# Performance work log

Hardware: AMD Instinct MI355X
Metric: run time of the kernel (lower is better)

Reference implementation:

```python
import jax, jax.numpy as jnp
import numpy as np
import math

B, S, D, H = 16, 1024, 1024, 16
HD = D // H                      # 64 head dim
MLP_H = int(int(D * 4.0) * 2 / 3)  # 2730 SwiGLU hidden
EPS = 1e-6


def _rmsnorm(h, w):
    # fp32 RMSNorm over last dim
    v = jnp.mean(h * h, axis=-1, keepdims=True)
    return w * (h * jax.lax.rsqrt(v + EPS))


def _rope(x):
    # x: [B, H, S, HD]; standard rotary, half-split convention
    hd = x.shape[-1]
    pos = jnp.arange(x.shape[-2], dtype=jnp.float32)
    inv = 1.0 / (10000.0 ** (jnp.arange(0, hd, 2, dtype=jnp.float32) / hd))
    fr = pos[:, None] * inv[None, :]          # [S, HD/2]
    cos, sin = jnp.cos(fr), jnp.sin(fr)
    x1, x2 = jnp.split(x, 2, axis=-1)
    return jnp.concatenate([x1 * cos - x2 * sin, x1 * sin + x2 * cos], axis=-1)


def setup_inputs() -> dict:
    key = jax.random.key(0)
    ks = jax.random.split(key, 16)
    sc = 0.02
    return {
        "x": jax.random.normal(ks[0], (B, S, D), jnp.float32),
        "c": jax.random.normal(ks[1], (B, D), jnp.float32),
        "w_qkv": jax.random.normal(ks[2], (D, 3 * D), jnp.float32) * sc,
        "b_qkv": jnp.zeros((3 * D,), jnp.float32),
        "w_proj": jax.random.normal(ks[3], (D, D), jnp.float32) * sc,
        "b_proj": jnp.zeros((D,), jnp.float32),
        "w12": jax.random.normal(ks[4], (D, 2 * MLP_H), jnp.float32) * sc,
        "b12": jnp.zeros((2 * MLP_H,), jnp.float32),
        "w3": jax.random.normal(ks[5], (MLP_H, D), jnp.float32) * sc,
        "b3": jnp.zeros((D,), jnp.float32),
        "w_ada": jax.random.normal(ks[6], (D, 6 * D), jnp.float32) * sc,
        "b_ada": jnp.zeros((6 * D,), jnp.float32),
        "norm1_w": jnp.ones((D,), jnp.float32),
        "norm2_w": jnp.ones((D,), jnp.float32),
        "qn_w": jnp.ones((HD,), jnp.float32),
        "kn_w": jnp.ones((HD,), jnp.float32),
    }


def _forward(x, c, w_qkv, b_qkv, w_proj, b_proj, w12, b12, w3, b3,
             w_ada, b_ada, norm1_w, norm2_w, qn_w, kn_w):
    # adaLN modulation params
    ada = jax.nn.silu(c) @ w_ada + b_ada               # [B, 6D]
    sh_a, sc_a, g_a, sh_m, sc_m, g_m = jnp.split(ada, 6, axis=-1)

    def modulate(h, shift, scale):
        return h * (1.0 + scale[:, None, :]) + shift[:, None, :]

    # --- attention branch ---
    h = modulate(_rmsnorm(x, norm1_w), sh_a, sc_a)     # [B, S, D]
    qkv = (h @ w_qkv + b_qkv).reshape(B, S, 3, H, HD)
    qkv = jnp.transpose(qkv, (2, 0, 3, 1, 4))          # [3, B, H, S, HD]
    q, k, v = qkv[0], qkv[1], qkv[2]
    q = _rope(_rmsnorm(q, qn_w))
    k = _rope(_rmsnorm(k, kn_w))
    scores = jnp.einsum('bhqd,bhkd->bhqk', q, k) / math.sqrt(HD)
    attn = jax.nn.softmax(scores, axis=-1)
    o = jnp.einsum('bhqk,bhkd->bhqd', attn, v)         # [B, H, S, HD]
    o = jnp.transpose(o, (0, 2, 1, 3)).reshape(B, S, D)
    o = o @ w_proj + b_proj
    x = x + g_a[:, None, :] * o

    # --- SwiGLU MLP branch ---
    h = modulate(_rmsnorm(x, norm2_w), sh_m, sc_m)
    x12 = h @ w12 + b12
    x1, x2 = jnp.split(x12, 2, axis=-1)
    mlp = (jax.nn.silu(x1) * x2) @ w3 + b3
    return x + g_m[:, None, :] * mlp


def reference(x, c, w_qkv, b_qkv, w_proj, b_proj, w12, b12, w3, b3,
              w_ada, b_ada, norm1_w, norm2_w, qn_w, kn_w):
    return _forward(x, c, w_qkv, b_qkv, w_proj, b_proj, w12, b12, w3, b3,
                    w_ada, b_ada, norm1_w, norm2_w, qn_w, kn_w)
```

## Files before the change

kernel.cpp:

```cpp
#include <hip/hip_runtime.h>
#include <hip/hip_bf16.h>
#include <math.h>

namespace {

constexpr int Bb = 16;
constexpr int Ss = 1024;
constexpr int Dd = 1024;
constexpr int Hh = 16;
constexpr int HD = 64;
constexpr int MLPH = 2730;
constexpr int MLPH_PAD = 2752;
constexpr int ADA_LD = 6144;
constexpr int NR = Bb * Ss;

typedef __attribute__((ext_vector_type(8))) short bf16x8;
typedef __attribute__((ext_vector_type(4))) float f32x4;
typedef __hip_bfloat16 bf16;
typedef unsigned int u32;

__device__ __forceinline__ float bf2f(bf16 v){ return __bfloat162float(v); }
__device__ __forceinline__ bf16 f2bf(float v){ return __float2bfloat16(v); }
__device__ __forceinline__ short f2bfs(float v){ bf16 t = __float2bfloat16(v); return __builtin_bit_cast(short, t); }

__device__ __forceinline__ f32x4 mfma16(bf16x8 a, bf16x8 b, f32x4 c){
  return __builtin_amdgcn_mfma_f32_16x16x32_bf16(a, b, c, 0, 0, 0);
}

__device__ __forceinline__ void gload16(const void* g, void* l){
  __builtin_amdgcn_global_load_lds(
      (const __attribute__((address_space(1))) u32*)g,
      (__attribute__((address_space(3))) u32*)l, 16, 0, 0);
}

__device__ __forceinline__ bf16x8 dsr128(const short* p){
  f32x4 r;
  asm volatile("ds_read_b128 %0, %1" : "=v"(r) : "v"((u32)(size_t)p));
  return __builtin_bit_cast(bf16x8, r);
}


__global__ void k_silu(const float* __restrict__ c, float* __restrict__ out, int n){
  int i = blockIdx.x*256 + threadIdx.x;
  if(i < n){ float v = c[i]; out[i] = v / (1.f + __expf(-v)); }
}

__global__ __launch_bounds__(256) void k_ada(const float* __restrict__ sc,
    const float* __restrict__ w, const float* __restrict__ bias, float* __restrict__ ada){
  __shared__ float red[4][Bb][64];
  int tid = threadIdx.x;
  int jj = tid & 63, ks = tid >> 6;
  int j = blockIdx.x*64 + jj;
  float acc[Bb];
  #pragma unroll
  for(int b=0;b<Bb;++b) acc[b] = 0.f;
  for(int k=ks*256; k<ks*256+256; ++k){
    float wv = w[(size_t)k*ADA_LD + j];
    #pragma unroll
    for(int b=0;b<Bb;++b) acc[b] += sc[b*Dd + k] * wv;
  }
  #pragma unroll
  for(int b=0;b<Bb;++b) red[ks][b][jj] = acc[b];
  __syncthreads();
  #pragma unroll
  for(int rep=0;rep<4;++rep){
    int idx = rep*256 + tid;
    int b = idx >> 6, j2 = idx & 63;
    float s = red[0][b][j2]+red[1][b][j2]+red[2][b][j2]+red[3][b][j2];
    ada[(size_t)b*ADA_LD + blockIdx.x*64 + j2] = s + bias[blockIdx.x*64 + j2];
  }
}

__global__ void k_rope_tab(float2* __restrict__ tab){
  int i = blockIdx.x*256 + threadIdx.x;
  int s = i >> 5, f = i & 31;
  float inv = powf(10000.f, -((float)(2*f)) / 64.f);
  float fr = (float)s * inv;
  float sv, cv;
  sincosf(fr, &sv, &cv);
  tab[i] = make_float2(cv, sv);
}

__global__ void k_transpose(const float* __restrict__ in, bf16* __restrict__ out,
                            int R, int C, int Rpad){
  __shared__ short tile[32][33];
  int tx = threadIdx.x & 31, ty = threadIdx.x >> 5;
  int tr0 = blockIdx.x*32, tc0 = blockIdx.y*32;
  #pragma unroll
  for(int i=0;i<4;++i){
    int r = tr0 + ty + i*8, cc = tc0 + tx;
    short v = 0;
    if(r < R && cc < C) v = f2bfs(in[(size_t)r*C + cc]);
    tile[ty+i*8][tx] = v;
  }
  __syncthreads();
  #pragma unroll
  for(int i=0;i<4;++i){
    int oc = tc0 + ty + i*8;
    int orow = tr0 + tx;
    if(oc < C && orow < Rpad)
      out[(size_t)oc*Rpad + orow] = __builtin_bit_cast(bf16, tile[tx][ty+i*8]);
  }
}

__global__ __launch_bounds__(256) void k_norm_mod(const float* __restrict__ x,
    const float* __restrict__ w, const float* __restrict__ shift, const float* __restrict__ scale,
    bf16* __restrict__ out){
  int r = blockIdx.x;
  int b = r >> 10;
  int t = threadIdx.x;
  const float* xr = x + (size_t)r*Dd;
  float v[4]; float ss = 0.f;
  #pragma unroll
  for(int i=0;i<4;++i){
    float f = xr[t*4+i];
    v[i] = f; ss += f*f;
  }
  #pragma unroll
  for(int m=1;m<64;m<<=1) ss += __shfl_xor(ss, m);
  __shared__ float red[4];
  if((t & 63) == 0) red[t>>6] = ss;
  __syncthreads();
  float tot = red[0]+red[1]+red[2]+red[3];
  float rms = rsqrtf(tot * (1.f/Dd) + 1e-6f);
  #pragma unroll
  for(int i=0;i<4;++i){
    int ccol = t*4+i;
    float h = v[i]*rms*w[ccol];
    float scv = scale[(size_t)b*ADA_LD + ccol];
    float shv = shift[(size_t)b*ADA_LD + ccol];
    out[(size_t)r*Dd + ccol] = f2bf(h*(1.f+scv) + shv);
  }
}

__global__ __launch_bounds__(256) void k_qknorm(bf16* __restrict__ qkv,
    const float* __restrict__ qw, const float* __restrict__ kw,
    const float2* __restrict__ tab){
  int bs = blockIdx.x;
  int s = bs & (Ss-1);
  int tid = threadIdx.x;
  int wv = tid >> 6, lane = tid & 63;
  int isK = wv >> 1;
  int chunk = (wv & 1)*64 + lane;
  int c = chunk & 7;
  int h = chunk >> 3;
  int dih = c*8;
  bf16* p = qkv + (size_t)bs*3072 + isK*Dd + h*HD + dih;
  bf16x8 v = *(const bf16x8*)p;
  float x[8]; float ss = 0.f;
  #pragma unroll
  for(int i=0;i<8;++i){ x[i] = bf2f(__builtin_bit_cast(bf16,(short)v[i])); ss += x[i]*x[i]; }
  ss += __shfl_xor(ss,1); ss += __shfl_xor(ss,2); ss += __shfl_xor(ss,4);
  float rms = rsqrtf(ss*(1.f/HD) + 1e-6f);
  const float* wn = isK ? kw : qw;
  float xn[8];
  #pragma unroll
  for(int i=0;i<8;++i) xn[i] = x[i]*rms*wn[dih+i];
  u32 pk[4], pq[4];
  #pragma unroll
  for(int i=0;i<4;++i)
    pk[i] = (u32)(unsigned short)f2bfs(xn[2*i]) |
            ((u32)(unsigned short)f2bfs(xn[2*i+1]) << 16);
  #pragma unroll
  for(int i=0;i<4;++i) pq[i] = __shfl_xor((int)pk[i], 4);
  float px[8];
  #pragma unroll
  for(int i=0;i<4;++i){
    px[2*i]   = bf2f(__builtin_bit_cast(bf16,(short)(pq[i] & 0xffff)));
    px[2*i+1] = bf2f(__builtin_bit_cast(bf16,(short)(pq[i] >> 16)));
  }
  const float2* tb = tab + s*32 + (c & 3)*8;
  float qs = isK ? 1.f : 0.18033688f;
  bf16x8 o;
  #pragma unroll
  for(int i=0;i<8;++i){
    float2 cs = tb[i];
    float r = (c < 4) ? (xn[i]*cs.x - px[i]*cs.y) : (px[i]*cs.y + xn[i]*cs.x);
    o[i] = f2bfs(r*qs);
  }
  *(bf16x8*)p = o;
}

#define LDA8(M,KH) dsr128(&Ah[((M)*16 + l15)*64 + ((((KH)*4 + l4) ^ l7))*8])
#define PHASE8(M0, STAGE_STMT, GATE_STMT) do{ \
  bf16x8 a0k0 = LDA8(M0,0), a0k1 = LDA8(M0,1), a1k0 = LDA8(M0+1,0), a1k1 = LDA8(M0+1,1); \
  STAGE_STMT; \
  __builtin_amdgcn_s_barrier(); \
  asm volatile("s_waitcnt lgkmcnt(0)" ::: "memory"); \
  __builtin_amdgcn_sched_barrier(0); \
  __builtin_amdgcn_s_setprio(1); \
  acc[M0][0]=mfma16(a0k0,bfrag[0][0],acc[M0][0]); \
  acc[M0][1]=mfma16(a0k0,bfrag[1][0],acc[M0][1]); \
  acc[M0][2]=mfma16(a0k0,bfrag[2][0],acc[M0][2]); \
  acc[M0][3]=mfma16(a0k0,bfrag[3][0],acc[M0][3]); \
  acc[M0+1][0]=mfma16(a1k0,bfrag[0][0],acc[M0+1][0]); \
  acc[M0+1][1]=mfma16(a1k0,bfrag[1][0],acc[M0+1][1]); \
  acc[M0+1][2]=mfma16(a1k0,bfrag[2][0],acc[M0+1][2]); \
  acc[M0+1][3]=mfma16(a1k0,bfrag[3][0],acc[M0+1][3]); \
  acc[M0][0]=mfma16(a0k1,bfrag[0][1],acc[M0][0]); \
  acc[M0][1]=mfma16(a0k1,bfrag[1][1],acc[M0][1]); \
  acc[M0][2]=mfma16(a0k1,bfrag[2][1],acc[M0][2]); \
  acc[M0][3]=mfma16(a0k1,bfrag[3][1],acc[M0][3]); \
  acc[M0+1][0]=mfma16(a1k1,bfrag[0][1],acc[M0+1][0]); \
  acc[M0+1][1]=mfma16(a1k1,bfrag[1][1],acc[M0+1][1]); \
  acc[M0+1][2]=mfma16(a1k1,bfrag[2][1],acc[M0+1][2]); \
  acc[M0+1][3]=mfma16(a1k1,bfrag[3][1],acc[M0+1][3]); \
  __builtin_amdgcn_s_setprio(0); \
  GATE_STMT; \
  __builtin_amdgcn_s_barrier(); }while(0)

template<int MODE>
__global__ __launch_bounds__(512, 2) void k_gemm8(
    const bf16* __restrict__ A, int lda,
    const bf16* __restrict__ BT, int ldb,
    const float* __restrict__ bias1, int K,
    const float* __restrict__ res, const float* __restrict__ gate,
    void* __restrict__ outp, int ldo)
{
  alignas(16) __shared__ short AH[2][2][128*64];
  alignas(16) __shared__ short BH[2][2][128*64];

  const int tid = threadIdx.x;
  const int lane = tid & 63, wid = tid >> 6;
  const int wm = wid >> 2, wn = wid & 3;
  const int l15 = lane & 15, l4 = lane >> 4;
  const int l7 = l15 & 7;
  const int brow = blockIdx.x * 256;
  const int bcol = blockIdx.y * 256;

  const int sr0 = tid >> 3;
  const int sr1 = sr0 + 64;
  const int sc  = ((tid & 7) ^ (sr0 & 7)) * 8;

  const bf16* Abase = A  + (size_t)brow*lda;
  const bf16* Bbase = BT + (size_t)bcol*ldb;

  auto stageA = [&](int t, int h){
    int d = t & 1;
    const bf16* g = Abase + (size_t)(h*128)*lda + t*64;
    gload16(g + (size_t)sr0*lda + sc, &AH[d][h][tid*8]);
    gload16(g + (size_t)sr1*lda + sc, &AH[d][h][(tid+512)*8]);
  };
  auto stageB = [&](int t, int h){
    int d = t & 1;
    const bf16* g = Bbase + (size_t)(h*128)*ldb + t*64;
    gload16(g + (size_t)sr0*ldb + sc, &BH[d][h][tid*8]);
    gload16(g + (size_t)sr1*ldb + sc, &BH[d][h][(tid+512)*8]);
  };

  f32x4 acc[8][4];
  f32x4 zero4 = {0.f,0.f,0.f,0.f};
  #pragma unroll
  for(int m=0;m<8;++m)
    #pragma unroll
    for(int n=0;n<4;++n) acc[m][n] = zero4;

  const int NT = K >> 6;
  stageA(0,0); stageA(0,1); stageB(0,0); stageB(0,1);
  stageB(1,0); stageB(1,1);
  asm volatile("s_waitcnt vmcnt(4)" ::: "memory");
  __builtin_amdgcn_sched_barrier(0);
  __builtin_amdgcn_s_barrier();

  const int bhsel = wn >> 1, brB = (wn & 1)*64;
  bf16x8 bfrag[4][2];

  for(int t=0; t<NT; ++t){
    const int d = t & 1;
    const short* Ah = AH[d][wm];
    const short* Bh = BH[d][bhsel];
    #pragma unroll
    for(int n=0;n<4;++n){
      int r = brB + n*16 + l15;
      bfrag[n][0] = dsr128(&Bh[r*64 + ((l4     ^ l7))*8]);
      bfrag[n][1] = dsr128(&Bh[r*64 + (((4|l4) ^ l7))*8]);
    }
    PHASE8(0, if(t+1 < NT) stageA(t+1,0), );
    PHASE8(2, if(t+1 < NT) stageA(t+1,1), );
    PHASE8(4, if(t+2 < NT) stageB(t+2,0), );
    PHASE8(6, if(t+2 < NT) stageB(t+2,1),
           asm volatile("s_waitcnt vmcnt(4)" ::: "memory");
           __builtin_amdgcn_sched_barrier(0) );
  }

  #pragma unroll
  for(int m=0;m<8;++m)
    #pragma unroll
    for(int n=0;n<4;++n)
      #pragma unroll
      for(int j=0;j<4;++j){
        int r  = brow + wm*128 + m*16 + l4*4 + j;
        int cc = bcol + wn*64  + n*16 + l15;
        float v = acc[m][n][j] + bias1[cc];
        if constexpr (MODE==0){
          ((bf16*)outp)[(size_t)r*ldo + cc] = f2bf(v);
        } else {
          int b = r >> 10;
          ((float*)outp)[(size_t)r*ldo + cc] =
              res[(size_t)r*Dd + cc] + gate[(size_t)b*ADA_LD + cc]*v;
        }
      }
}

__global__ __launch_bounds__(256, 2) void k_gemm3(
    const bf16* __restrict__ A, int lda,
    const bf16* __restrict__ BT, long long b2off, int ldb,
    const float* __restrict__ bias1, const float* __restrict__ bias2,
    int K, bf16* __restrict__ outp, int ldo)
{
  alignas(16) __shared__ short As[3][128*32];
  alignas(16) __shared__ short Bs[3][64*32];
  alignas(16) __shared__ short Bs2[3][64*32];

  int tid = threadIdx.x;
  int lane = tid & 63, wid = tid >> 6;
  int wm = wid >> 1, wn = wid & 1;
  int l15 = lane & 15, l4 = lane >> 4;
  int brow = blockIdx.x * 128;
  int bcol = blockIdx.y * 64;

  int r0 = tid >> 2, s0 = tid & 3;
  int r1 = r0 + 64;
  int k80 = s0 ^ ((r0 >> 1) & 3);
  int k81 = s0 ^ ((r1 >> 1) & 3);

  const bf16* a0 = A  + (size_t)(brow+r0)*lda + k80*8;
  const bf16* a1 = A  + (size_t)(brow+r1)*lda + k81*8;
  const bf16* b0 = BT + (size_t)(bcol+r0)*ldb + k80*8;

  f32x4 zero4 = {0.f,0.f,0.f,0.f};
  f32x4 acc[4][2], acc2[4][2];
  #pragma unroll
  for(int m=0;m<4;++m)
    #pragma unroll
    for(int n=0;n<2;++n){ acc[m][n]=zero4; acc2[m][n]=zero4; }

  auto STAGE = [&](int kt, int bi){
    int ko = kt << 5;
    gload16(a0 + ko, &As[bi][tid*8]);
    gload16(a1 + ko, &As[bi][(tid+256)*8]);
    gload16(b0 + ko, &Bs[bi][tid*8]);
    gload16(b0 + b2off + ko, &Bs2[bi][tid*8]);
  };

  const int nk = K >> 5;
  STAGE(0, 0);
  STAGE(1, 1);
  asm volatile("s_waitcnt vmcnt(4)" ::: "memory");
  __builtin_amdgcn_sched_barrier(0);
  __builtin_amdgcn_s_barrier();

  int arr[4], asl[4];
  #pragma unroll
  for(int m=0;m<4;++m){
    arr[m] = wm*64 + m*16 + l15;
    asl[m] = l4 ^ ((arr[m] >> 1) & 3);
  }
  int brr[2], bsl[2];
  #pragma unroll
  for(int n=0;n<2;++n){
    brr[n] = wn*32 + n*16 + l15;
    bsl[n] = l4 ^ ((brr[n] >> 1) & 3);
  }

  int bi = 0;
  for(int kt=0; kt<nk; ++kt){
    bool more = (kt+2) < nk;
    int bn = bi+2; if(bn >= 3) bn -= 3;
    if(more) STAGE(kt+2, bn);

    bf16x8 af[4], bfr[2], bfr2[2];
    #pragma unroll
    for(int m=0;m<4;++m) af[m] = dsr128(&As[bi][arr[m]*32 + asl[m]*8]);
    #pragma unroll
    for(int n=0;n<2;++n){
      bfr[n]  = dsr128(&Bs[bi][brr[n]*32 + bsl[n]*8]);
      bfr2[n] = dsr128(&Bs2[bi][brr[n]*32 + bsl[n]*8]);
    }
    asm volatile("s_waitcnt lgkmcnt(0)" ::: "memory");
    __builtin_amdgcn_sched_barrier(0);
    __builtin_amdgcn_s_setprio(1);
    #pragma unroll
    for(int m=0;m<4;++m){
      acc[m][0]  = mfma16(af[m], bfr[0],  acc[m][0]);
      acc2[m][0] = mfma16(af[m], bfr2[0], acc2[m][0]);
      acc[m][1]  = mfma16(af[m], bfr[1],  acc[m][1]);
      acc2[m][1] = mfma16(af[m], bfr2[1], acc2[m][1]);
    }
    __builtin_amdgcn_s_setprio(0);
    if(more){ asm volatile("s_waitcnt vmcnt(4)" ::: "memory"); }
    else    { asm volatile("s_waitcnt vmcnt(0)" ::: "memory"); }
    __builtin_amdgcn_sched_barrier(0);
    __builtin_amdgcn_s_barrier();
    ++bi; if(bi >= 3) bi = 0;
  }

  #pragma unroll
  for(int m=0;m<4;++m)
    #pragma unroll
    for(int n=0;n<2;++n)
      #pragma unroll
      for(int j=0;j<4;++j){
        int r  = brow + wm*64 + m*16 + l4*4 + j;
        int cc = bcol + wn*32 + n*16 + l15;
        float o = 0.f;
        if(cc < MLPH){
          float v1 = acc[m][n][j] + bias1[cc];
          float v2 = acc2[m][n][j] + bias2[cc];
          o = (v1/(1.f+__expf(-v1)))*v2;
        }
        outp[(size_t)r*ldo + cc] = f2bf(o);
      }
}

__global__ __launch_bounds__(256) void k_attn(const bf16* __restrict__ qkv, bf16* __restrict__ obuf){
  alignas(16) __shared__ short Ks[64*64];
  alignas(16) __shared__ short VTs[64*64];
  alignas(16) __shared__ short Ps[128*64];

  int flatb = blockIdx.x;
  int low3 = flatb & 7;
  int rest = flatb >> 3;
  int qb   = rest & 7;
  int bh   = ((rest >> 3) << 3) | low3;
  int b = bh >> 4, h = bh & 15;

  int tid = threadIdx.x;
  int lane = tid & 63, w = tid >> 6;
  int l15 = lane & 15, l4 = lane >> 4;

  const bf16* base = qkv + (size_t)b*Ss*3072 + h*HD;

  bf16x8 aq[2][2];
  #pragma unroll
  for(int hi=0;hi<2;++hi)
    #pragma unroll
    for(int hf=0;hf<2;++hf)
      aq[hi][hf] = *(const bf16x8*)(base +
          (size_t)(qb*128 + w*32 + hi*16 + l15)*3072 + hf*32 + l4*8);

  int r0 = tid >> 3, c0 = tid & 7;
  int khcol = (c0 ^ (r0 & 7)) * 8;
  bf16x8 kreg[2], vreg[2];
  #pragma unroll
  for(int ch=0; ch<2; ++ch){
    int rr = r0 + ch*32;
    kreg[ch] = *(const bf16x8*)(base + Dd   + (size_t)rr*3072 + khcol);
    vreg[ch] = *(const bf16x8*)(base + 2*Dd + (size_t)rr*3072 + c0*8);
  }

  f32x4 zero4 = {0.f,0.f,0.f,0.f};
  f32x4 acc_o[2][4];
  float mrow[2], lrow[2];
  #pragma unroll
  for(int hi=0;hi<2;++hi){
    mrow[hi] = -1e30f; lrow[hi] = 0.f;
    #pragma unroll
    for(int an=0;an<4;++an) acc_o[hi][an] = zero4;
  }

  const float THR = 11.54f;

  for(int kb=0; kb<Ss/64; ++kb){
    if(kb) __syncthreads();
    #pragma unroll
    for(int ch=0; ch<2; ++ch){
      *(bf16x8*)&Ks[(tid + ch*256)*8] = kreg[ch];
      int vr = r0 + ch*32;
      #pragma unroll
      for(int i=0;i<8;++i){
        int g = i ^ c0;
        VTs[(c0*8 + i)*64 + (vr ^ (g<<3))] = vreg[ch][i];
      }
    }
    if(kb+1 < Ss/64){
      #pragma unroll
      for(int ch=0; ch<2; ++ch){
        int rr = (kb+1)*64 + r0 + ch*32;
        kreg[ch] = *(const bf16x8*)(base + Dd   + (size_t)rr*3072 + khcol);
        vreg[ch] = *(const bf16x8*)(base + 2*Dd + (size_t)rr*3072 + c0*8);
      }
    }
    __syncthreads();

    bf16x8 kf[4][2];
    #pragma unroll
    for(int an=0;an<4;++an){
      int R = an*16 + l15;
      kf[an][0] = *(const bf16x8*)&Ks[R*64 + ((l4     ^ (R&7)))*8];
      kf[an][1] = *(const bf16x8*)&Ks[R*64 + (((4|l4) ^ (R&7)))*8];
    }
    f32x4 sacc[2][4];
    #pragma unroll
    for(int hi=0;hi<2;++hi)
      #pragma unroll
      for(int an=0;an<4;++an) sacc[hi][an] = zero4;
    __builtin_amdgcn_s_setprio(1);
    #pragma unroll
    for(int an=0;an<4;++an){
      sacc[0][an] = mfma16(kf[an][0], aq[0][0], sacc[0][an]);
      sacc[1][an] = mfma16(kf[an][0], aq[1][0], sacc[1][an]);
    }
    #pragma unroll
    for(int an=0;an<4;++an){
      sacc[0][an] = mfma16(kf[an][1], aq[0][1], sacc[0][an]);
      sacc[1][an] = mfma16(kf[an][1], aq[1][1], sacc[1][an]);
    }
    __builtin_amdgcn_s_setprio(0);

    #pragma unroll
    for(int hi=0; hi<2; ++hi){
      float mx = -1e30f;
      #pragma unroll
      for(int an=0;an<4;++an)
        #pragma unroll
        for(int j=0;j<4;++j) mx = fmaxf(mx, sacc[hi][an][j]);
      mx = fmaxf(mx, __shfl_xor(mx, 16));
      mx = fmaxf(mx, __shfl_xor(mx, 32));
      bool grow = mx > mrow[hi] + THR;
      if(__any(grow)){
        float mnew = fmaxf(mrow[hi], mx);
        float corr = exp2f(mrow[hi] - mnew);
        mrow[hi] = mnew;
        lrow[hi] *= corr;
        float cj[4];
        #pragma unroll
        for(int j=0;j<4;++j) cj[j] = __shfl(corr, l4*4 + j);
        #pragma unroll
        for(int an=0;an<4;++an)
          #pragma unroll
          for(int j=0;j<4;++j) acc_o[hi][an][j] *= cj[j];
      }
      float psum = 0.f;
      #pragma unroll
      for(int an=0;an<4;++an)
        #pragma unroll
        for(int j=0;j<4;++j){
          float pv = exp2f(sacc[hi][an][j] - mrow[hi]);
          sacc[hi][an][j] = pv; psum += pv;
        }
      psum += __shfl_xor(psum, 16);
      psum += __shfl_xor(psum, 32);
      lrow[hi] += psum;

      int prow = w*32 + hi*16 + l15;
      int pg = (l15 & 7) << 3;
      #pragma unroll
      for(int an=0;an<4;++an)
        #pragma unroll
        for(int j=0;j<4;++j)
          Ps[prow*64 + ((an*16 + l4*4 + j) ^ pg)] = f2bfs(sacc[hi][an][j]);
    }

    int pgme = (l15 & 7) << 3;
    bf16x8 pa[2][2];
    #pragma unroll
    for(int hi=0;hi<2;++hi){
      int prow = w*32 + hi*16 + l15;
      pa[hi][0] = *(const bf16x8*)&Ps[prow*64 + ((l4*8)      ^ pgme)];
      pa[hi][1] = *(const bf16x8*)&Ps[prow*64 + ((32 + l4*8) ^ pgme)];
    }
    bf16x8 vf[4][2];
    #pragma unroll
    for(int an2=0;an2<4;++an2){
      int dR = an2*16 + l15;
      int g = ((dR & 7) ^ ((dR >> 3) & 7)) << 3;
      vf[an2][0] = *(const bf16x8*)&VTs[dR*64 + ((l4*8)      ^ g)];
      vf[an2][1] = *(const bf16x8*)&VTs[dR*64 + ((32 + l4*8) ^ g)];
    }
    __builtin_amdgcn_s_setprio(1);
    #pragma unroll
    for(int an2=0;an2<4;++an2){
      acc_o[0][an2] = mfma16(pa[0][0], vf[an2][0], acc_o[0][an2]);
      acc_o[1][an2] = mfma16(pa[1][0], vf[an2][0], acc_o[1][an2]);
    }
    #pragma unroll
    for(int an2=0;an2<4;++an2){
      acc_o[0][an2] = mfma16(pa[0][1], vf[an2][1], acc_o[0][an2]);
      acc_o[1][an2] = mfma16(pa[1][1], vf[an2][1], acc_o[1][an2]);
    }
    __builtin_amdgcn_s_setprio(0);
  }

  #pragma unroll
  for(int hi=0;hi<2;++hi){
    float lr[4];
    #pragma unroll
    for(int j=0;j<4;++j) lr[j] = __shfl(lrow[hi], l4*4 + j);
    #pragma unroll
    for(int an2=0;an2<4;++an2)
      #pragma unroll
      for(int j=0;j<4;++j){
        int r = qb*128 + w*32 + hi*16 + l4*4 + j;
        float ov = acc_o[hi][an2][j] / lr[j];
        obuf[((size_t)b*Ss + r)*Dd + h*HD + an2*16 + l15] = f2bf(ov);
      }
  }
}

}

extern "C" void kernel_launch(void* const* d_in, const int* in_sizes, int n_in,
                              void* d_out, int out_size, void* d_ws, size_t ws_size,
                              hipStream_t stream){
  const float* x      = (const float*)d_in[0];
  const float* c      = (const float*)d_in[1];
  const float* w_qkv  = (const float*)d_in[2];
  const float* b_qkv  = (const float*)d_in[3];
  const float* w_proj = (const float*)d_in[4];
  const float* b_proj = (const float*)d_in[5];
  const float* w12    = (const float*)d_in[6];
  const float* b12    = (const float*)d_in[7];
  const float* w3     = (const float*)d_in[8];
  const float* b3     = (const float*)d_in[9];
  const float* w_ada  = (const float*)d_in[10];
  const float* b_ada  = (const float*)d_in[11];
  const float* n1w    = (const float*)d_in[12];
  const float* n2w    = (const float*)d_in[13];
  const float* qnw    = (const float*)d_in[14];
  const float* knw    = (const float*)d_in[15];
  float* out = (float*)d_out;
  (void)in_sizes; (void)n_in; (void)out_size;

  constexpr size_t WS_NEED = 227254272ull;
  if (ws_size < WS_NEED) return;

  char* ws = (char*)d_ws;
  float*  silu_c = (float*)(ws + 0);
  float*  ada    = (float*)(ws + 65536);
  float2* ropet  = (float2*)(ws + 458752);
  bf16*   wqkvT  = (bf16*)(ws + 720896);
  bf16*   wprojT = (bf16*)(ws + 7012352);
  bf16*   w12T   = (bf16*)(ws + 9109504);
  bf16*   w3T    = (bf16*)(ws + 20291584);
  bf16*   hbuf   = (bf16*)(ws + 25927680);
  bf16*   qkvb   = (bf16*)(ws + 59482112);
  float*  xmid   = (float*)(ws + 160145408);
  bf16*   obuf   = hbuf;
  bf16*   h2     = hbuf;
  bf16*   mlpmid = qkvb;

  k_silu<<<64,256,0,stream>>>(c, silu_c, Bb*Dd);
  k_rope_tab<<<128,256,0,stream>>>(ropet);
  k_ada<<<96,256,0,stream>>>(silu_c, w_ada, b_ada, ada);
  k_transpose<<<dim3(32,96),256,0,stream>>>(w_qkv, wqkvT, 1024, 3072, 1024);
  k_transpose<<<dim3(32,32),256,0,stream>>>(w_proj, wprojT, 1024, 1024, 1024);
  k_transpose<<<dim3(32,171),256,0,stream>>>(w12, w12T, 1024, 5460, 1024);
  k_transpose<<<dim3(86,32),256,0,stream>>>(w3, w3T, 2730, 1024, 2752);

  k_norm_mod<<<NR,256,0,stream>>>(x, n1w, ada + 0, ada + 1024, hbuf);
  k_gemm8<0><<<dim3(64,12),512,0,stream>>>(hbuf,1024, wqkvT,1024,
      b_qkv, 1024, nullptr,nullptr, qkvb,3072);
  k_qknorm<<<NR,256,0,stream>>>(qkvb, qnw, knw, ropet);
  k_attn<<<2048,256,0,stream>>>(qkvb, obuf);
  k_gemm8<1><<<dim3(64,4),512,0,stream>>>(obuf,1024, wprojT,1024,
      b_proj, 1024, x, ada + 2048, xmid,1024);

  k_norm_mod<<<NR,256,0,stream>>>(xmid, n2w, ada + 3072, ada + 4096, h2);
  k_gemm3<<<dim3(128,43),256,0,stream>>>(h2,1024, w12T,(long long)MLPH*1024,1024,
      b12, b12 + MLPH, 1024, mlpmid, MLPH_PAD);
  k_gemm8<1><<<dim3(64,4),512,0,stream>>>(mlpmid,MLPH_PAD, w3T,MLPH_PAD,
      b3, MLPH_PAD, xmid, ada + 5120, out,1024);
}
```

Before: 863.2 us.

## Deepen SwiGLU GEMM pipeline to four LDS stages with register double-buffering

The fused w12/SwiGLU GEMM kernel grows from three to four shared-memory stages, so global loads are issued three K-tiles ahead instead of two. It also double-buffers the MFMA operand fragments in registers: the LDS reads for the next tile are issued before the MFMAs on the current tile, and the loop is unrolled by two to swap the fragment sets. The goal is to hide both global-load and LDS-read latency behind the matrix core work. The cost is 64KB of LDS per block and more registers, which may limit occupancy under the (256,2) launch bounds. The unrolled loop also assumes an even number of K-tiles.

```diff
diff --git a/kernel.cpp b/kernel.cpp
--- a/kernel.cpp
+++ b/kernel.cpp
@@ -308,9 +308,9 @@
     const float* __restrict__ bias1, const float* __restrict__ bias2,
     int K, bf16* __restrict__ outp, int ldo)
 {
-  alignas(16) __shared__ short As[3][128*32];
-  alignas(16) __shared__ short Bs[3][64*32];
-  alignas(16) __shared__ short Bs2[3][64*32];
+  alignas(16) __shared__ short As[4][128*32];
+  alignas(16) __shared__ short Bs[4][64*32];
+  alignas(16) __shared__ short Bs2[4][64*32];
 
   int tid = threadIdx.x;
   int lane = tid & 63, wid = tid >> 6;
@@ -343,57 +343,72 @@
     gload16(b0 + b2off + ko, &Bs2[bi][tid*8]);
   };
 
+  int arr[4], asl[4];
+  #pragma unroll
+  for(int m=0;m<4;++m){
+    arr[m] = wm*64 + m*16 + l15;
+    asl[m] = l4 ^ ((arr[m] >> 1) & 3);
+  }
+  int brr[2], bsl[2];
+  #pragma unroll
+  for(int n=0;n<2;++n){
+    brr[n] = wn*32 + n*16 + l15;
+    bsl[n] = l4 ^ ((brr[n] >> 1) & 3);
+  }
+
   const int nk = K >> 5;
-  STAGE(0, 0);
-  STAGE(1, 1);
+  STAGE(0, 0); STAGE(1, 1); STAGE(2, 2);
   asm volatile("s_waitcnt vmcnt(4)" ::: "memory");
   __builtin_amdgcn_sched_barrier(0);
   __builtin_amdgcn_s_barrier();
 
-  int arr[4], asl[4];
-  #pragma unroll
-  for(int m=0;m<4;++m){
-    arr[m] = wm*64 + m*16 + l15;
-    asl[m] = l4 ^ ((arr[m] >> 1) & 3);
-  }
-  int brr[2], bsl[2];
+  bf16x8 afA[4], bfrA[2], bfr2A[2];
+  bf16x8 afB[4], bfrB[2], bfr2B[2];
+
+  #pragma unroll
+  for(int m=0;m<4;++m) afA[m] = dsr128(&As[0][arr[m]*32 + asl[m]*8]);
   #pragma unroll
   for(int n=0;n<2;++n){
-    brr[n] = wn*32 + n*16 + l15;
-    bsl[n] = l4 ^ ((brr[n] >> 1) & 3);
-  }
-
-  int bi = 0;
-  for(int kt=0; kt<nk; ++kt){
-    bool more = (kt+2) < nk;
-    int bn = bi+2; if(bn >= 3) bn -= 3;
-    if(more) STAGE(kt+2, bn);
-
-    bf16x8 af[4], bfr[2], bfr2[2];
-    #pragma unroll
-    for(int m=0;m<4;++m) af[m] = dsr128(&As[bi][arr[m]*32 + asl[m]*8]);
-    #pragma unroll
-    for(int n=0;n<2;++n){
-      bfr[n]  = dsr128(&Bs[bi][brr[n]*32 + bsl[n]*8]);
-      bfr2[n] = dsr128(&Bs2[bi][brr[n]*32 + bsl[n]*8]);
-    }
-    asm volatile("s_waitcnt lgkmcnt(0)" ::: "memory");
-    __builtin_amdgcn_sched_barrier(0);
-    __builtin_amdgcn_s_setprio(1);
-    #pragma unroll
-    for(int m=0;m<4;++m){
-      acc[m][0]  = mfma16(af[m], bfr[0],  acc[m][0]);
-      acc2[m][0] = mfma16(af[m], bfr2[0], acc2[m][0]);
-      acc[m][1]  = mfma16(af[m], bfr[1],  acc[m][1]);
-      acc2[m][1] = mfma16(af[m], bfr2[1], acc2[m][1]);
-    }
-    __builtin_amdgcn_s_setprio(0);
-    if(more){ asm volatile("s_waitcnt vmcnt(4)" ::: "memory"); }
-    else    { asm volatile("s_waitcnt vmcnt(0)" ::: "memory"); }
-    __builtin_amdgcn_sched_barrier(0);
-    __builtin_amdgcn_s_barrier();
-    ++bi; if(bi >= 3) bi = 0;
-  }
+    bfrA[n]  = dsr128(&Bs[0][brr[n]*32 + bsl[n]*8]);
+    bfr2A[n] = dsr128(&Bs2[0][brr[n]*32 + bsl[n]*8]);
+  }
+  asm volatile("s_waitcnt lgkmcnt(0)" ::: "memory");
+  __builtin_amdgcn_sched_barrier(0);
+
+#define G3_BODY(T, afC, bfrC, bfr2C, afN, bfrN, bfr2N) do{                 \
+    if((T)+3 < nk) STAGE((T)+3, ((T)+3)&3);                                \
+    if((T)+1 < nk){                                                        \
+      const int nb = ((T)+1)&3;                                            \
+      _Pragma("unroll")                                                    \
+      for(int m=0;m<4;++m) afN[m] = dsr128(&As[nb][arr[m]*32 + asl[m]*8]); \
+      _Pragma("unroll")                                                    \
+      for(int n=0;n<2;++n){                                                \
+        bfrN[n]  = dsr128(&Bs[nb][brr[n]*32 + bsl[n]*8]);                  \
+        bfr2N[n] = dsr128(&Bs2[nb][brr[n]*32 + bsl[n]*8]);                 \
+      }                                                                    \
+    }                                                                      \
+    __builtin_amdgcn_s_setprio(1);                                         \
+    _Pragma("unroll")                                                      \
+    for(int m=0;m<4;++m){                                                  \
+      acc[m][0]  = mfma16(afC[m], bfrC[0],  acc[m][0]);                    \
+      acc2[m][0] = mfma16(afC[m], bfr2C[0], acc2[m][0]);                   \
+      acc[m][1]  = mfma16(afC[m], bfrC[1],  acc[m][1]);                    \
+      acc2[m][1] = mfma16(afC[m], bfr2C[1], acc2[m][1]);                   \
+    }                                                                      \
+    __builtin_amdgcn_s_setprio(0);                                         \
+    asm volatile("s_waitcnt lgkmcnt(0)" ::: "memory");                     \
+    __builtin_amdgcn_sched_barrier(0);                                     \
+    if((T)+3 < nk){ asm volatile("s_waitcnt vmcnt(4)" ::: "memory"); }     \
+    else          { asm volatile("s_waitcnt vmcnt(0)" ::: "memory"); }     \
+    __builtin_amdgcn_sched_barrier(0);                                     \
+    __builtin_amdgcn_s_barrier();                                          \
+  }while(0)
+
+  for(int t=0; t<nk; t+=2){
+    G3_BODY(t,   afA, bfrA, bfr2A, afB, bfrB, bfr2B);
+    G3_BODY(t+1, afB, bfrB, bfr2B, afA, bfrA, bfr2A);
+  }
+#undef G3_BODY
 
   #pragma unroll
   for(int m=0;m<4;++m)
```

After: 889.7 us. +3.1%, slower.
